# Performance work log

Hardware: AMD Instinct MI355X
Metric: run time of the kernel (lower is better)

## Reference

```python
import jax, jax.numpy as jnp
import numpy as np

_B, _H, _W = 4, 352, 1216
_N = 400000
_CIN, _CHID, _COUT = 64, 16, 64
_EPS = 1e-5


def setup_inputs() -> dict:
    key = jax.random.key(0)
    ks = jax.random.split(key, 12)
    pc_features = jax.random.normal(ks[0], (_N, _CIN), dtype=jnp.float32)
    # Pinhole intrinsics, identical per batch image (KITTI-like)
    fx = fy = 500.0
    cx, cy = _W / 2.0, _H / 2.0
    K0 = jnp.array([[fx, 0.0, cx], [0.0, fy, cy], [0.0, 0.0, 1.0]], dtype=jnp.float32)
    cam = jnp.tile(K0[None], (_B, 1, 1))
    # Sample uniform pixel coords + depth, back-project so projection is uniform over the image
    u = jax.random.uniform(ks[1], (_N,), minval=0.0, maxval=_W - 1.0)
    v = jax.random.uniform(ks[2], (_N,), minval=0.0, maxval=_H - 1.0)
    z = jax.random.uniform(ks[3], (_N,), minval=1.0, maxval=50.0)
    x = (u - cx) * z / fx
    y = (v - cy) * z / fy
    pc_pos = jnp.stack([x, y, z], axis=-1).astype(jnp.float32)
    pc_batch = jax.random.randint(ks[4], (_N,), 0, _B, dtype=jnp.int32)
    # MLP([64, 16, 64]) params
    W1 = jax.random.normal(ks[5], (_CIN, _CHID), dtype=jnp.float32) / np.sqrt(_CIN)
    b1 = jnp.zeros((_CHID,), dtype=jnp.float32)
    W2 = jax.random.normal(ks[6], (_CHID, _COUT), dtype=jnp.float32) / np.sqrt(_CHID)
    b2 = jnp.zeros((_COUT,), dtype=jnp.float32)
    zero_encoding = 0.02 * jax.random.normal(ks[7], (1, _COUT), dtype=jnp.float32)
    gamma = jnp.ones((_COUT,), dtype=jnp.float32)
    beta = jnp.zeros((_COUT,), dtype=jnp.float32)
    return {
        'pc_features': pc_features, 'pc_pos': pc_pos, 'pc_batch': pc_batch, 'cam': cam,
        'W1': W1, 'b1': b1, 'W2': W2, 'b2': b2, 'zero_encoding': zero_encoding,
        'gamma': gamma, 'beta': beta, 'B': _B, 'H': _H, 'W': _W,
    }


def reference(pc_features, pc_pos, pc_batch, cam, W1, b1, W2, b2, zero_encoding, gamma, beta, B, H, W):
    # MLP projection of per-point features: 64 -> 16 -> 64
    feats = jax.nn.relu(pc_features @ W1 + b1) @ W2 + b2  # [N, C]
    C = feats.shape[1]
    # project_pc: pinhole projection of points into the image grid
    Kp = cam[pc_batch]                                    # [N, 3, 3]
    p = jnp.einsum('nij,nj->ni', Kp, pc_pos)              # [N, 3]
    u = p[:, 0] / p[:, 2]
    v = p[:, 1] / p[:, 2]
    ui = jnp.clip(jnp.floor(u), 0, W - 1).astype(jnp.int32)
    vi = jnp.clip(jnp.floor(v), 0, H - 1).astype(jnp.int32)
    flat_idx = pc_batch * (H * W) + vi * W + ui           # [N]
    # Grid initialized with learned zero_encoding (pixels without points keep it),
    # then point features scattered at their projected pixel locations.
    grid = jnp.broadcast_to(zero_encoding, (B * H * W, C))
    grid = grid.at[flat_idx].set(feats)
    grid = grid.reshape(B, H, W, C).transpose(0, 3, 1, 2)  # [B, C, H, W]
    # BatchNorm2d (training mode: batch statistics over B,H,W)
    mean = grid.mean(axis=(0, 2, 3), keepdims=True)
    var = grid.var(axis=(0, 2, 3), keepdims=True)
    out = (grid - mean) * jax.lax.rsqrt(var + _EPS)
    out = out * gamma.reshape(1, -1, 1, 1) + beta.reshape(1, -1, 1, 1)
    return out
```

## Files before the change

kernel.cpp:

```cpp
#include <hip/hip_runtime.h>
#include <math.h>

#define TPB   256
#define CIN   64
#define CHID  16
#define COUT  64
#define BB    4
#define HH    352
#define WW    1216
#define HW_   (HH * WW)
#define MTOT  (BB * HW_)
#define NCOPY 32
#define WTILES (WW / 64)
#define NTILES (BB * HH * WTILES)
#define KS_BLOCKS 768


__global__ __launch_bounds__(TPB) void k_init(int4* __restrict__ winner4,
                                              float4* __restrict__ statsf4,
                                              int* __restrict__ count) {
    int g = blockIdx.x * TPB + threadIdx.x;
    if (g < MTOT / 4) winner4[g] = make_int4(-1, -1, -1, -1);
    if (g < (NCOPY * 128) / 4) statsf4[g] = make_float4(0.f, 0.f, 0.f, 0.f);
    if (g == 0) *count = 0;
}

__global__ __launch_bounds__(TPB) void k_project(const float* __restrict__ pos,
                                                 const int* __restrict__ batch,
                                                 const float* __restrict__ cam,
                                                 int N,
                                                 int* __restrict__ winner,
                                                 int* __restrict__ pixarr) {
    int n = blockIdx.x * TPB + threadIdx.x;
    if (n >= N) return;
    int b = batch[n];
    const float* Km = cam + b * 9;
    float x = pos[3 * n + 0];
    float y = pos[3 * n + 1];
    float z = pos[3 * n + 2];
    float p0 = __fadd_rn(__fadd_rn(__fmul_rn(Km[0], x), __fmul_rn(Km[1], y)),
                         __fmul_rn(Km[2], z));
    float p1 = __fadd_rn(__fadd_rn(__fmul_rn(Km[3], x), __fmul_rn(Km[4], y)),
                         __fmul_rn(Km[5], z));
    float p2 = __fadd_rn(__fadd_rn(__fmul_rn(Km[6], x), __fmul_rn(Km[7], y)),
                         __fmul_rn(Km[8], z));
    float u = __fdiv_rn(p0, p2);
    float v = __fdiv_rn(p1, p2);
    float uf = fminf(fmaxf(floorf(u), 0.0f), (float)(WW - 1));
    float vf = fminf(fmaxf(floorf(v), 0.0f), (float)(HH - 1));
    int ui = (int)uf;
    int vi = (int)vf;
    int p = b * HW_ + vi * WW + ui;
    pixarr[n] = p;
    atomicMax(&winner[p], n);
}

__global__ __launch_bounds__(TPB) void k_hid(const float* __restrict__ feat,
        const float* __restrict__ W1, const float* __restrict__ b1,
        const int* __restrict__ winner, const int* __restrict__ pixarr,
        int N, float* __restrict__ hidw, int* __restrict__ count) {
    int n = blockIdx.x * TPB + threadIdx.x;
    if (n >= N) return;
    bool active = (winner[pixarr[n]] == n);
    unsigned long long mb = __ballot(active);
    if ((threadIdx.x & 63) == 0) atomicAdd(count, (int)__popcll(mb));

    float h[CHID];
#pragma unroll
    for (int k = 0; k < CHID; k++) h[k] = b1[k];
    const float4* X = (const float4*)(feat + (size_t)n * CIN);
    const float4* W14 = (const float4*)W1;
#pragma unroll
    for (int j4 = 0; j4 < 16; j4++) {
        float4 x4 = X[j4];
#pragma unroll
        for (int e = 0; e < 4; e++) {
            int j = 4 * j4 + e;
            float xj = (e == 0) ? x4.x : (e == 1) ? x4.y : (e == 2) ? x4.z : x4.w;
#pragma unroll
            for (int m = 0; m < 4; m++) {
                float4 w = W14[j * 4 + m];
                h[4 * m + 0] = fmaf(xj, w.x, h[4 * m + 0]);
                h[4 * m + 1] = fmaf(xj, w.y, h[4 * m + 1]);
                h[4 * m + 2] = fmaf(xj, w.z, h[4 * m + 2]);
                h[4 * m + 3] = fmaf(xj, w.w, h[4 * m + 3]);
            }
        }
    }
    float4* Ho = (float4*)(hidw + (size_t)n * CHID);
#pragma unroll
    for (int m = 0; m < 4; m++) {
        float4 o;
        o.x = active ? fmaxf(h[4 * m + 0], 0.f) : 0.f;
        o.y = active ? fmaxf(h[4 * m + 1], 0.f) : 0.f;
        o.z = active ? fmaxf(h[4 * m + 2], 0.f) : 0.f;
        o.w = active ? fmaxf(h[4 * m + 3], 0.f) : 0.f;
        Ho[m] = o;
    }
}

__global__ __launch_bounds__(TPB) void k_sums(const float* __restrict__ hidw,
        const float* __restrict__ W2, int N, float* __restrict__ statsf) {
    int c = threadIdx.x & 63;
    int wv = blockIdx.x * (TPB / 64) + (threadIdx.x >> 6);
    wv = __builtin_amdgcn_readfirstlane(wv);
    float w2c[CHID];
#pragma unroll
    for (int h = 0; h < CHID; h++) w2c[h] = W2[h * COUT + c];
    const int TW = KS_BLOCKS * (TPB / 64);
    int chunk = (N + TW - 1) / TW;
    int i0 = wv * chunk;
    int i1 = min(N, i0 + chunk);
    float s = 0.f, q = 0.f;
    for (int i = i0; i < i1; i++) {
        const float4* Hp = (const float4*)(hidw + (size_t)i * CHID);
        float g = 0.f;
#pragma unroll
        for (int m = 0; m < 4; m++) {
            float4 hv = Hp[m];
            g = fmaf(hv.x, w2c[4 * m + 0], g);
            g = fmaf(hv.y, w2c[4 * m + 1], g);
            g = fmaf(hv.z, w2c[4 * m + 2], g);
            g = fmaf(hv.w, w2c[4 * m + 3], g);
        }
        s += g;
        q = fmaf(g, g, q);
    }
    float* dst = statsf + (wv & (NCOPY - 1)) * 128;
    atomicAdd(&dst[c], s);
    atomicAdd(&dst[64 + c], q);
}

__global__ __launch_bounds__(64) void k_finalize(const float* __restrict__ statsf,
        const int* __restrict__ count, const float* __restrict__ W2,
        const float* __restrict__ b2, const float* __restrict__ zenc,
        const float* __restrict__ gmm, const float* __restrict__ bta,
        float* __restrict__ w2tp, float* __restrict__ biasp,
        float* __restrict__ emptyv) {
    int c = threadIdx.x;
    float S1 = 0.f, S2 = 0.f;
    for (int g = 0; g < NCOPY; g++) {
        S1 += statsf[g * 128 + c];
        S2 += statsf[g * 128 + 64 + c];
    }
    float K = (float)(*count);
    float b2c = b2[c];
    float sumf  = K * b2c + S1;
    float sumsq = fmaf(K * b2c, b2c, fmaf(2.f * b2c, S1, S2));
    const float Mf = (float)MTOT;
    float zc = zenc[c];
    float mean = (sumf + (Mf - K) * zc) / Mf;
    float e2   = (sumsq + (Mf - K) * zc * zc) / Mf;
    float var  = e2 - mean * mean;
    float inv  = 1.0f / sqrtf(var + 1e-5f);
    float sc = gmm[c] * inv;
    float sh = bta[c] - mean * sc;
    emptyv[c] = fmaf(zc, sc, sh);
    biasp[c]  = fmaf(b2c, sc, sh);
    for (int h = 0; h < CHID; h++) w2tp[c * CHID + h] = W2[h * COUT + c] * sc;
}

__global__ __launch_bounds__(TPB) void k_out(const float* __restrict__ hidw,
        const int* __restrict__ winner, const float* __restrict__ w2tp,
        const float* __restrict__ biasp, const float* __restrict__ emptyv,
        float* __restrict__ out) {
    int tile = blockIdx.x * (TPB / 64) + (threadIdx.x >> 6);
    tile = __builtin_amdgcn_readfirstlane(tile);
    int p = threadIdx.x & 63;
    int wt  = tile % WTILES;
    int rem = tile / WTILES;
    int hh  = rem % HH;
    int bb  = rem / HH;
    int pix0 = bb * HW_ + hh * WW + wt * 64;

    int n = winner[pix0 + p];
    bool act = (n >= 0);
    size_t nn = act ? (size_t)n : 0;
    const float4* Hp = (const float4*)(hidw + nn * CHID);
    float4 h0 = Hp[0], h1 = Hp[1], h2 = Hp[2], h3 = Hp[3];

    float* ob = out + (size_t)bb * ((size_t)COUT * HW_) + (size_t)hh * WW + wt * 64 + p;
    const float4* W4 = (const float4*)w2tp;
#pragma unroll 4
    for (int c = 0; c < COUT; c++) {
        float4 wa = W4[c * 4 + 0];
        float4 wb = W4[c * 4 + 1];
        float4 wc = W4[c * 4 + 2];
        float4 wd = W4[c * 4 + 3];
        float f = biasp[c];
        f = fmaf(h0.x, wa.x, f); f = fmaf(h0.y, wa.y, f);
        f = fmaf(h0.z, wa.z, f); f = fmaf(h0.w, wa.w, f);
        f = fmaf(h1.x, wb.x, f); f = fmaf(h1.y, wb.y, f);
        f = fmaf(h1.z, wb.z, f); f = fmaf(h1.w, wb.w, f);
        f = fmaf(h2.x, wc.x, f); f = fmaf(h2.y, wc.y, f);
        f = fmaf(h2.z, wc.z, f); f = fmaf(h2.w, wc.w, f);
        f = fmaf(h3.x, wd.x, f); f = fmaf(h3.y, wd.y, f);
        f = fmaf(h3.z, wd.z, f); f = fmaf(h3.w, wd.w, f);
        float ev = emptyv[c];
        ob[(size_t)c * HW_] = act ? f : ev;
    }
}

extern "C" void kernel_launch(void* const* d_in, const int* in_sizes, int n_in,
                              void* d_out, int out_size, void* d_ws, size_t ws_size,
                              hipStream_t stream) {
    const float* feat  = (const float*)d_in[0];
    const float* pos   = (const float*)d_in[1];
    const int*   batch = (const int*)d_in[2];
    const float* cam   = (const float*)d_in[3];
    const float* W1    = (const float*)d_in[4];
    const float* b1    = (const float*)d_in[5];
    const float* W2    = (const float*)d_in[6];
    const float* b2    = (const float*)d_in[7];
    const float* zenc  = (const float*)d_in[8];
    const float* gmm   = (const float*)d_in[9];
    const float* bta   = (const float*)d_in[10];
    int N = in_sizes[2];

    int*   winner = (int*)d_ws;
    int*   pixarr = winner + MTOT;
    float* statsf = (float*)(pixarr + N);
    int*   misc   = (int*)(statsf + NCOPY * 128);
    float* hidw   = (float*)(misc + 4);
    float* w2tp   = hidw + (size_t)N * CHID;
    float* biasp  = w2tp + COUT * CHID;
    float* emptyv = biasp + COUT;
    int*   count  = misc;
    float* outp   = (float*)d_out;

    k_init<<<MTOT / 4 / TPB, TPB, 0, stream>>>((int4*)winner, (float4*)statsf, count);
    k_project<<<(N + TPB - 1) / TPB, TPB, 0, stream>>>(pos, batch, cam, N, winner, pixarr);
    k_hid<<<(N + TPB - 1) / TPB, TPB, 0, stream>>>(feat, W1, b1, winner, pixarr, N, hidw, count);
    k_sums<<<KS_BLOCKS, TPB, 0, stream>>>(hidw, W2, N, statsf);
    k_finalize<<<1, 64, 0, stream>>>(statsf, count, W2, b2, zenc, gmm, bta,
                                     w2tp, biasp, emptyv);
    k_out<<<NTILES / (TPB / 64), TPB, 0, stream>>>(hidw, winner, w2tp, biasp, emptyv, outp);
}
```

Measured before the change: 676.1 us.

## Store hidden activations as bf16 and use nontemporal loads/stores

Packs the 16-wide ReLU hidden vector into bf16 (round-to-nearest-even) instead of fp32, halving the intermediate buffer read by the stats kernel and gathered by the output kernel. It also adds nontemporal loads for the input features and nontemporal stores for the large output tensor to reduce cache pollution. The cost is reduced precision in the hidden activations, which may affect the final outputs and the batch statistics.

```diff
diff --git a/kernel.cpp b/kernel.cpp
--- a/kernel.cpp
+++ b/kernel.cpp
@@ -15,6 +15,15 @@
 #define NTILES (BB * HH * WTILES)
 #define KS_BLOCKS 768
 
+typedef float f32x4 __attribute__((ext_vector_type(4)));
+
+
+__device__ __forceinline__ unsigned bf16rne(float x) {
+    unsigned u = __float_as_uint(x);
+    return (u + 0x7fffu + ((u >> 16) & 1u)) >> 16;
+}
+__device__ __forceinline__ float bflo(unsigned u) { return __uint_as_float(u << 16); }
+__device__ __forceinline__ float bfhi(unsigned u) { return __uint_as_float(u & 0xffff0000u); }
 
 __global__ __launch_bounds__(TPB) void k_init(int4* __restrict__ winner4,
                                               float4* __restrict__ statsf4,
@@ -58,7 +67,7 @@
 __global__ __launch_bounds__(TPB) void k_hid(const float* __restrict__ feat,
         const float* __restrict__ W1, const float* __restrict__ b1,
         const int* __restrict__ winner, const int* __restrict__ pixarr,
-        int N, float* __restrict__ hidw, int* __restrict__ count) {
+        int N, unsigned* __restrict__ hidb, int* __restrict__ count) {
     int n = blockIdx.x * TPB + threadIdx.x;
     if (n >= N) return;
     bool active = (winner[pixarr[n]] == n);
@@ -68,38 +77,42 @@
     float h[CHID];
 #pragma unroll
     for (int k = 0; k < CHID; k++) h[k] = b1[k];
-    const float4* X = (const float4*)(feat + (size_t)n * CIN);
-    const float4* W14 = (const float4*)W1;
+    const f32x4* X = (const f32x4*)(feat + (size_t)n * CIN);
+    const f32x4* W14 = (const f32x4*)W1;
 #pragma unroll
     for (int j4 = 0; j4 < 16; j4++) {
-        float4 x4 = X[j4];
+        f32x4 x4 = __builtin_nontemporal_load(&X[j4]);
 #pragma unroll
         for (int e = 0; e < 4; e++) {
             int j = 4 * j4 + e;
-            float xj = (e == 0) ? x4.x : (e == 1) ? x4.y : (e == 2) ? x4.z : x4.w;
+            float xj = x4[e];
 #pragma unroll
             for (int m = 0; m < 4; m++) {
-                float4 w = W14[j * 4 + m];
-                h[4 * m + 0] = fmaf(xj, w.x, h[4 * m + 0]);
-                h[4 * m + 1] = fmaf(xj, w.y, h[4 * m + 1]);
-                h[4 * m + 2] = fmaf(xj, w.z, h[4 * m + 2]);
-                h[4 * m + 3] = fmaf(xj, w.w, h[4 * m + 3]);
+                f32x4 w = W14[j * 4 + m];
+                h[4 * m + 0] = fmaf(xj, w[0], h[4 * m + 0]);
+                h[4 * m + 1] = fmaf(xj, w[1], h[4 * m + 1]);
+                h[4 * m + 2] = fmaf(xj, w[2], h[4 * m + 2]);
+                h[4 * m + 3] = fmaf(xj, w[3], h[4 * m + 3]);
             }
         }
     }
-    float4* Ho = (float4*)(hidw + (size_t)n * CHID);
-#pragma unroll
-    for (int m = 0; m < 4; m++) {
-        float4 o;
-        o.x = active ? fmaxf(h[4 * m + 0], 0.f) : 0.f;
-        o.y = active ? fmaxf(h[4 * m + 1], 0.f) : 0.f;
-        o.z = active ? fmaxf(h[4 * m + 2], 0.f) : 0.f;
-        o.w = active ? fmaxf(h[4 * m + 3], 0.f) : 0.f;
-        Ho[m] = o;
-    }
-}
-
-__global__ __launch_bounds__(TPB) void k_sums(const float* __restrict__ hidw,
+#pragma unroll
+    for (int k = 0; k < CHID; k++) h[k] = active ? fmaxf(h[k], 0.f) : 0.f;
+    uint4 o0, o1;
+    o0.x = bf16rne(h[0])  | (bf16rne(h[1])  << 16);
+    o0.y = bf16rne(h[2])  | (bf16rne(h[3])  << 16);
+    o0.z = bf16rne(h[4])  | (bf16rne(h[5])  << 16);
+    o0.w = bf16rne(h[6])  | (bf16rne(h[7])  << 16);
+    o1.x = bf16rne(h[8])  | (bf16rne(h[9])  << 16);
+    o1.y = bf16rne(h[10]) | (bf16rne(h[11]) << 16);
+    o1.z = bf16rne(h[12]) | (bf16rne(h[13]) << 16);
+    o1.w = bf16rne(h[14]) | (bf16rne(h[15]) << 16);
+    uint4* Ho = (uint4*)(hidb + (size_t)n * 8);
+    Ho[0] = o0;
+    Ho[1] = o1;
+}
+
+__global__ __launch_bounds__(TPB) void k_sums(const unsigned* __restrict__ hidb,
         const float* __restrict__ W2, int N, float* __restrict__ statsf) {
     int c = threadIdx.x & 63;
     int wv = blockIdx.x * (TPB / 64) + (threadIdx.x >> 6);
@@ -113,16 +126,17 @@
     int i1 = min(N, i0 + chunk);
     float s = 0.f, q = 0.f;
     for (int i = i0; i < i1; i++) {
-        const float4* Hp = (const float4*)(hidw + (size_t)i * CHID);
+        const uint4* Hp = (const uint4*)(hidb + (size_t)i * 8);
+        uint4 A = Hp[0], B = Hp[1];
         float g = 0.f;
-#pragma unroll
-        for (int m = 0; m < 4; m++) {
-            float4 hv = Hp[m];
-            g = fmaf(hv.x, w2c[4 * m + 0], g);
-            g = fmaf(hv.y, w2c[4 * m + 1], g);
-            g = fmaf(hv.z, w2c[4 * m + 2], g);
-            g = fmaf(hv.w, w2c[4 * m + 3], g);
-        }
+        g = fmaf(bflo(A.x), w2c[0],  g); g = fmaf(bfhi(A.x), w2c[1],  g);
+        g = fmaf(bflo(A.y), w2c[2],  g); g = fmaf(bfhi(A.y), w2c[3],  g);
+        g = fmaf(bflo(A.z), w2c[4],  g); g = fmaf(bfhi(A.z), w2c[5],  g);
+        g = fmaf(bflo(A.w), w2c[6],  g); g = fmaf(bfhi(A.w), w2c[7],  g);
+        g = fmaf(bflo(B.x), w2c[8],  g); g = fmaf(bfhi(B.x), w2c[9],  g);
+        g = fmaf(bflo(B.y), w2c[10], g); g = fmaf(bfhi(B.y), w2c[11], g);
+        g = fmaf(bflo(B.z), w2c[12], g); g = fmaf(bfhi(B.z), w2c[13], g);
+        g = fmaf(bflo(B.w), w2c[14], g); g = fmaf(bfhi(B.w), w2c[15], g);
         s += g;
         q = fmaf(g, g, q);
     }
@@ -160,7 +174,7 @@
     for (int h = 0; h < CHID; h++) w2tp[c * CHID + h] = W2[h * COUT + c] * sc;
 }
 
-__global__ __launch_bounds__(TPB) void k_out(const float* __restrict__ hidw,
+__global__ __launch_bounds__(TPB) void k_out(const unsigned* __restrict__ hidb,
         const int* __restrict__ winner, const float* __restrict__ w2tp,
         const float* __restrict__ biasp, const float* __restrict__ emptyv,
         float* __restrict__ out) {
@@ -176,28 +190,37 @@
     int n = winner[pix0 + p];
     bool act = (n >= 0);
     size_t nn = act ? (size_t)n : 0;
-    const float4* Hp = (const float4*)(hidw + nn * CHID);
-    float4 h0 = Hp[0], h1 = Hp[1], h2 = Hp[2], h3 = Hp[3];
+    const uint4* Hp = (const uint4*)(hidb + nn * 8);
+    uint4 A = Hp[0], B = Hp[1];
+    float hv[CHID];
+    hv[0]  = bflo(A.x); hv[1]  = bfhi(A.x);
+    hv[2]  = bflo(A.y); hv[3]  = bfhi(A.y);
+    hv[4]  = bflo(A.z); hv[5]  = bfhi(A.z);
+    hv[6]  = bflo(A.w); hv[7]  = bfhi(A.w);
+    hv[8]  = bflo(B.x); hv[9]  = bfhi(B.x);
+    hv[10] = bflo(B.y); hv[11] = bfhi(B.y);
+    hv[12] = bflo(B.z); hv[13] = bfhi(B.z);
+    hv[14] = bflo(B.w); hv[15] = bfhi(B.w);
 
     float* ob = out + (size_t)bb * ((size_t)COUT * HW_) + (size_t)hh * WW + wt * 64 + p;
-    const float4* W4 = (const float4*)w2tp;
+    const f32x4* W4 = (const f32x4*)w2tp;
 #pragma unroll 4
     for (int c = 0; c < COUT; c++) {
-        float4 wa = W4[c * 4 + 0];
-        float4 wb = W4[c * 4 + 1];
-        float4 wc = W4[c * 4 + 2];
-        float4 wd = W4[c * 4 + 3];
+        f32x4 wa = W4[c * 4 + 0];
+        f32x4 wb = W4[c * 4 + 1];
+        f32x4 wc = W4[c * 4 + 2];
+        f32x4 wd = W4[c * 4 + 3];
         float f = biasp[c];
-        f = fmaf(h0.x, wa.x, f); f = fmaf(h0.y, wa.y, f);
-        f = fmaf(h0.z, wa.z, f); f = fmaf(h0.w, wa.w, f);
-        f = fmaf(h1.x, wb.x, f); f = fmaf(h1.y, wb.y, f);
-        f = fmaf(h1.z, wb.z, f); f = fmaf(h1.w, wb.w, f);
-        f = fmaf(h2.x, wc.x, f); f = fmaf(h2.y, wc.y, f);
-        f = fmaf(h2.z, wc.z, f); f = fmaf(h2.w, wc.w, f);
-        f = fmaf(h3.x, wd.x, f); f = fmaf(h3.y, wd.y, f);
-        f = fmaf(h3.z, wd.z, f); f = fmaf(h3.w, wd.w, f);
+        f = fmaf(hv[0],  wa[0], f); f = fmaf(hv[1],  wa[1], f);
+        f = fmaf(hv[2],  wa[2], f); f = fmaf(hv[3],  wa[3], f);
+        f = fmaf(hv[4],  wb[0], f); f = fmaf(hv[5],  wb[1], f);
+        f = fmaf(hv[6],  wb[2], f); f = fmaf(hv[7],  wb[3], f);
+        f = fmaf(hv[8],  wc[0], f); f = fmaf(hv[9],  wc[1], f);
+        f = fmaf(hv[10], wc[2], f); f = fmaf(hv[11], wc[3], f);
+        f = fmaf(hv[12], wd[0], f); f = fmaf(hv[13], wd[1], f);
+        f = fmaf(hv[14], wd[2], f); f = fmaf(hv[15], wd[3], f);
         float ev = emptyv[c];
-        ob[(size_t)c * HW_] = act ? f : ev;
+        __builtin_nontemporal_store(act ? f : ev, ob + (size_t)c * HW_);
     }
 }
 
@@ -217,22 +240,22 @@
     const float* bta   = (const float*)d_in[10];
     int N = in_sizes[2];
 
-    int*   winner = (int*)d_ws;
-    int*   pixarr = winner + MTOT;
-    float* statsf = (float*)(pixarr + N);
-    int*   misc   = (int*)(statsf + NCOPY * 128);
-    float* hidw   = (float*)(misc + 4);
-    float* w2tp   = hidw + (size_t)N * CHID;
-    float* biasp  = w2tp + COUT * CHID;
-    float* emptyv = biasp + COUT;
-    int*   count  = misc;
-    float* outp   = (float*)d_out;
+    int*      winner = (int*)d_ws;
+    int*      pixarr = winner + MTOT;
+    float*    statsf = (float*)(pixarr + N);
+    int*      misc   = (int*)(statsf + NCOPY * 128);
+    unsigned* hidb   = (unsigned*)(misc + 4);
+    float*    w2tp   = (float*)(hidb + (size_t)N * 8);
+    float*    biasp  = w2tp + COUT * CHID;
+    float*    emptyv = biasp + COUT;
+    int*      count  = misc;
+    float*    outp   = (float*)d_out;
 
     k_init<<<MTOT / 4 / TPB, TPB, 0, stream>>>((int4*)winner, (float4*)statsf, count);
     k_project<<<(N + TPB - 1) / TPB, TPB, 0, stream>>>(pos, batch, cam, N, winner, pixarr);
-    k_hid<<<(N + TPB - 1) / TPB, TPB, 0, stream>>>(feat, W1, b1, winner, pixarr, N, hidw, count);
-    k_sums<<<KS_BLOCKS, TPB, 0, stream>>>(hidw, W2, N, statsf);
+    k_hid<<<(N + TPB - 1) / TPB, TPB, 0, stream>>>(feat, W1, b1, winner, pixarr, N, hidb, count);
+    k_sums<<<KS_BLOCKS, TPB, 0, stream>>>(hidb, W2, N, statsf);
     k_finalize<<<1, 64, 0, stream>>>(statsf, count, W2, b2, zenc, gmm, bta,
                                      w2tp, biasp, emptyv);
-    k_out<<<NTILES / (TPB / 64), TPB, 0, stream>>>(hidw, winner, w2tp, biasp, emptyv, outp);
-}
+    k_out<<<NTILES / (TPB / 64), TPB, 0, stream>>>(hidb, winner, w2tp, biasp, emptyv, outp);
+}
```

Result: no change. 669.4 us (-1.0%).
